# Performance work log

Measured on AMD Instinct MI355X. Metric: run time of the kernel, lower is better.

## Reference

```python
import jax, jax.numpy as jnp
import numpy as np

DIM = 96
HEADS = 3
WS = (2, 7, 7)   # window (Wt, Wh, Ww)
SS = (1, 3, 3)   # shift (St, Sh, Sw)
MLP_H = 4 * DIM
B, T, H, W = 1, 16, 112, 112
EPS = 1e-5


def _partition(x, ws):
    # (b,t,h,w,c) -> (b * t/Wt * h/Wh * w/Ww, Wt*Wh*Ww, c); works for np and jnp
    b, t, h, w, c = x.shape
    Wt, Wh, Ww = ws
    x = x.reshape(b, t // Wt, Wt, h // Wh, Wh, w // Ww, Ww, c)
    return x.transpose(0, 1, 3, 5, 2, 4, 6, 7).reshape(-1, Wt * Wh * Ww, c)


def _reverse(win, ws, b, t, h, w):
    Wt, Wh, Ww = ws
    c = win.shape[-1]
    x = win.reshape(b, t // Wt, h // Wh, w // Ww, Wt, Wh, Ww, c)
    return x.transpose(0, 1, 4, 2, 5, 3, 6, 7).reshape(b, t, h, w, c)


def _rel_pos_index(ws):
    Wt, Wh, Ww = ws
    coords = np.stack(np.meshgrid(np.arange(Wt), np.arange(Wh), np.arange(Ww), indexing='ij'))
    cf = coords.reshape(3, -1)
    rel = (cf[:, :, None] - cf[:, None, :]).transpose(1, 2, 0).astype(np.int64)
    rel[..., 0] += Wt - 1
    rel[..., 1] += Wh - 1
    rel[..., 2] += Ww - 1
    rel[..., 0] *= (2 * Wh - 1) * (2 * Ww - 1)
    rel[..., 1] *= 2 * Ww - 1
    return jnp.asarray(rel.sum(-1))  # (N, N)


def _attn_mask(tp, hp, wp, ws, ss):
    img = np.zeros((1, tp, hp, wp, 1), np.float32)
    cnt = 0
    def sl(Wd, Sd):
        return (slice(0, -Wd), slice(-Wd, -Sd), slice(-Sd, None))
    for ts in sl(ws[0], ss[0]):
        for hs in sl(ws[1], ss[1]):
            for wws in sl(ws[2], ss[2]):
                img[:, ts, hs, wws, :] = cnt
                cnt += 1
    mw = _partition(img, ws)[..., 0]                 # (nW, N)
    am = mw[:, None, :] - mw[:, :, None]
    return jnp.asarray(np.where(am != 0, -100.0, 0.0).astype(np.float32))


def _ln(x, g, b):
    m = x.mean(-1, keepdims=True)
    v = ((x - m) ** 2).mean(-1, keepdims=True)
    return (x - m) * jax.lax.rsqrt(v + EPS) * g + b


def setup_inputs() -> dict:
    key = jax.random.key(0)
    ks = jax.random.split(key, 8)
    Wt, Wh, Ww = WS
    n_bias = (2 * Wt - 1) * (2 * Wh - 1) * (2 * Ww - 1)
    s = 0.02
    return {
        'x': jax.random.normal(ks[0], (B, T, H, W, DIM), jnp.float32),
        'g1': jnp.ones((DIM,), jnp.float32),
        'b1': jnp.zeros((DIM,), jnp.float32),
        'qkv_w': jax.random.normal(ks[1], (DIM, 3 * DIM), jnp.float32) * s,
        'qkv_b': jnp.zeros((3 * DIM,), jnp.float32),
        'rpb': jax.random.normal(ks[2], (n_bias, HEADS), jnp.float32) * s,
        'proj_w': jax.random.normal(ks[3], (DIM, DIM), jnp.float32) * s,
        'proj_b': jnp.zeros((DIM,), jnp.float32),
        'g2': jnp.ones((DIM,), jnp.float32),
        'b2': jnp.zeros((DIM,), jnp.float32),
        'fc1_w': jax.random.normal(ks[4], (DIM, MLP_H), jnp.float32) * s,
        'fc1_b': jnp.zeros((MLP_H,), jnp.float32),
        'fc2_w': jax.random.normal(ks[5], (MLP_H, DIM), jnp.float32) * s,
        'fc2_b': jnp.zeros((DIM,), jnp.float32),
    }


def reference(x, g1, b1, qkv_w, qkv_b, rpb, proj_w, proj_b, g2, b2, fc1_w, fc1_b, fc2_w, fc2_b):
    Wt, Wh, Ww = WS
    St, Sh, Sw = SS
    Bx, Tx, Hx, Wx, C = x.shape
    N = Wt * Wh * Ww
    hd = C // HEADS
    shortcut = x
    xn = _ln(x, g1, b1)
    xs = jnp.roll(xn, (-St, -Sh, -Sw), axis=(1, 2, 3))
    xw = _partition(xs, WS)                           # (B_, N, C)
    B_ = xw.shape[0]
    nW = B_ // Bx
    qkv = (xw @ qkv_w + qkv_b).reshape(B_, N, 3, HEADS, hd).transpose(2, 0, 3, 1, 4)
    q, k, v = qkv[0] * (hd ** -0.5), qkv[1], qkv[2]   # (B_, H, N, hd)
    attn = jnp.einsum('bhnd,bhmd->bhnm', q, k)
    ridx = _rel_pos_index(WS)
    bias = rpb[ridx.reshape(-1)].reshape(N, N, HEADS).transpose(2, 0, 1)
    attn = attn + bias[None]
    mask = _attn_mask(Tx, Hx, Wx, WS, SS)             # (nW, N, N)
    attn = attn.reshape(Bx, nW, HEADS, N, N) + mask[None, :, None]
    attn = jax.nn.softmax(attn.reshape(B_, HEADS, N, N), axis=-1)
    out = jnp.einsum('bhnm,bhmd->bhnd', attn, v).transpose(0, 2, 1, 3).reshape(B_, N, C)
    out = out @ proj_w + proj_b
    xr = _reverse(out, WS, Bx, Tx, Hx, Wx)
    xr = jnp.roll(xr, (St, Sh, Sw), axis=(1, 2, 3))
    x1 = shortcut + xr
    xn2 = _ln(x1, g2, b2)
    h1 = jax.nn.gelu(xn2 @ fc1_w + fc1_b, approximate=False)
    return x1 + h1 @ fc2_w + fc2_b
```

## Files before the change

kernel.cpp:

```cpp
#include <hip/hip_runtime.h>
#include <math.h>

#define TT 16
#define HH 112
#define WD 112
#define CC 96
#define NHEADS 3
#define HD 32
#define NN 98
#define NWIN 2048
#define NTOK 200704
#define MLPH 384
#define SXP 104
#define SQP 40
#define SVP 136
#define SHP 392
#define SX1P 100

typedef unsigned int  u32;
typedef unsigned short u16;
typedef float f32x4 __attribute__((ext_vector_type(4)));
typedef short bf16x8 __attribute__((ext_vector_type(8)));

__device__ inline u16 f2bf(float f) {
  u32 u = __float_as_uint(f);
  u += 0x7fffu + ((u >> 16) & 1u);
  return (u16)(u >> 16);
}
__device__ inline float bflo(u32 u) { return __uint_as_float(u << 16); }
__device__ inline float bfhi(u32 u) { return __uint_as_float(u & 0xffff0000u); }

#define MFMA16(a, b, c) __builtin_amdgcn_mfma_f32_16x16x32_bf16((a), (b), (c), 0, 0, 0)

__global__ __launch_bounds__(256) void wprep_kernel(
    const float* __restrict__ qkv_w, const float* __restrict__ proj_w,
    const float* __restrict__ fc1_w, const float* __restrict__ fc2_w,
    u16* __restrict__ qkv_wT, u16* __restrict__ proj_wT,
    u16* __restrict__ fc1_wT, u16* __restrict__ fc2_wT) {
  int idx = blockIdx.x * 256 + threadIdx.x;
  if (idx < 27648) {
    int col = idx / CC, c = idx - col * CC;
    qkv_wT[idx] = f2bf(qkv_w[c * (3 * CC) + col]);
    return;
  }
  idx -= 27648;
  if (idx < 9216) {
    int col = idx / CC, c = idx - col * CC;
    proj_wT[idx] = f2bf(proj_w[c * CC + col]);
    return;
  }
  idx -= 9216;
  if (idx < 36864) {
    int j = idx / CC, c = idx - j * CC;
    fc1_wT[idx] = f2bf(fc1_w[c * MLPH + j]);
    return;
  }
  idx -= 36864;
  if (idx < 36864) {
    int c = idx / MLPH, j = idx - c * MLPH;
    fc2_wT[idx] = f2bf(fc2_w[j * CC + c]);
  }
}

__global__ __launch_bounds__(256) void bias_kernel(const float* __restrict__ rpb,
                                                   float* __restrict__ biasTP) {
  int idx = blockIdx.x * 256 + threadIdx.x;
  if (idx >= NHEADS * 112 * 128) return;
  int head = idx / (112 * 128);
  int r = idx - head * 112 * 128;
  int q = r / 128, kv = r - q * 128;
  float v;
  if (kv >= NN) v = -30000.f;
  else if (q >= NN) v = 0.f;
  else {
    int itq = q / 49, rq = q - itq * 49, ihq = rq / 7, iwq = rq - ihq * 7;
    int itk = kv / 49, rk = kv - itk * 49, ihk = rk / 7, iwk = rk - ihk * 7;
    int ridx = (itq - itk + 1) * 169 + (ihq - ihk + 6) * 13 + (iwq - iwk + 6);
    v = rpb[ridx * NHEADS + head];
  }
  biasTP[idx] = v;
}

__global__ __launch_bounds__(256) void ln1_kernel(
    const float* __restrict__ x, const float* __restrict__ g1, const float* __restrict__ b1,
    u16* __restrict__ xnw)
{
  const int tid = threadIdx.x;
  const int row = blockIdx.x * 64 + (tid >> 2);
  const int qd = tid & 3;
  const int widx = row / 112;
  const int n = row - widx * 112;
  u16* dst = xnw + (size_t)row * CC + qd * 24;
  if (n >= NN) {
    uint4 z = {0u, 0u, 0u, 0u};
    *(uint4*)(dst) = z; *(uint4*)(dst + 8) = z; *(uint4*)(dst + 16) = z;
    return;
  }
  int it = n / 49, r = n - it * 49, ih = r / 7, iw = r - ih * 7;
  int ww = widx & 15, hw = (widx >> 4) & 15, tw = widx >> 8;
  int t = tw * 2 + it + 1; if (t >= TT) t -= TT;
  int h = hw * 7 + ih + 3; if (h >= HH) h -= HH;
  int w = ww * 7 + iw + 3; if (w >= WD) w -= WD;
  const float* src = x + ((size_t)(t * HH + h) * WD + w) * CC + qd * 24;
  float v[24];
  #pragma unroll
  for (int i = 0; i < 24; i += 4) {
    float4 f = *(const float4*)(src + i);
    v[i] = f.x; v[i + 1] = f.y; v[i + 2] = f.z; v[i + 3] = f.w;
  }
  float sm = 0.f;
  #pragma unroll
  for (int i = 0; i < 24; ++i) sm += v[i];
  sm += __shfl_xor(sm, 1, 64);
  sm += __shfl_xor(sm, 2, 64);
  float mu = sm * (1.f / CC);
  float sq = 0.f;
  #pragma unroll
  for (int i = 0; i < 24; ++i) { float d = v[i] - mu; sq += d * d; }
  sq += __shfl_xor(sq, 1, 64);
  sq += __shfl_xor(sq, 2, 64);
  float inv = rsqrtf(sq * (1.f / CC) + 1e-5f);
  u16 o[24];
  #pragma unroll
  for (int i = 0; i < 24; ++i) {
    int c = qd * 24 + i;
    o[i] = f2bf((v[i] - mu) * inv * g1[c] + b1[c]);
  }
  *(uint4*)(dst)      = *(const uint4*)(o);
  *(uint4*)(dst + 8)  = *(const uint4*)(o + 8);
  *(uint4*)(dst + 16) = *(const uint4*)(o + 16);
}

__global__ __launch_bounds__(256, 4) void attn_kernel(
    const u16* __restrict__ xnw, const u16* __restrict__ qkv_wT, const float* __restrict__ qkv_b,
    const float* __restrict__ biasTP, u16* __restrict__ att)
{
  __shared__ __align__(16) u16 sUni[112 * SVP];
  __shared__ __align__(16) u16 sVt[32 * SVP];
  __shared__ int sReg[112];

  u16* sQ = sUni;
  u16* sK = sUni + 112 * SQP;
  u16* sP = sUni;

  const int tid  = threadIdx.x;
  const int bid  = blockIdx.x;
  const int widx = bid / 3;
  const int head = bid - widx * 3;
  const int ww = widx & 15, hw = (widx >> 4) & 15, tw = widx >> 8;
  const bool bnd = (tw == 7) || (hw == 15) || (ww == 15);
  const int wid = tid >> 6;
  const int lane = tid & 63;
  const int g  = lane >> 4;
  const int cl = lane & 15;
  const int mt1ok = (wid + 4) < 7;

  bf16x8 xa[2][3];
  {
    const u16* arow0 = xnw + ((size_t)widx * 112 + wid * 16 + cl) * CC + 8 * g;
    xa[0][0] = *(const bf16x8*)(arow0);
    xa[0][1] = *(const bf16x8*)(arow0 + 32);
    xa[0][2] = *(const bf16x8*)(arow0 + 64);
    const int mtb = mt1ok ? (wid + 4) : wid;
    const u16* arow1 = xnw + ((size_t)widx * 112 + mtb * 16 + cl) * CC + 8 * g;
    xa[1][0] = *(const bf16x8*)(arow1);
    xa[1][1] = *(const bf16x8*)(arow1 + 32);
    xa[1][2] = *(const bf16x8*)(arow1 + 64);
  }

  for (int i = tid; i < 32 * SVP / 2; i += 256) ((u32*)sVt)[i] = 0;
  if (tid < 112) {
    int n = tid;
    int reg = 0;
    if (n < NN) {
      int it = n / 49, r = n - it * 49, ih = r / 7, iw = r - ih * 7;
      int ts = tw * 2 + it, hs = hw * 7 + ih, ws2 = ww * 7 + iw;
      int rt = ts < TT - 2 ? 0 : (ts < TT - 1 ? 1 : 2);
      int rh = hs < HH - 7 ? 0 : (hs < HH - 3 ? 1 : 2);
      int rw = ws2 < WD - 7 ? 0 : (ws2 < WD - 3 ? 1 : 2);
      reg = rt * 9 + rh * 3 + rw;
    }
    sReg[n] = reg;
  }
  __syncthreads();

  {
    const float scale = 0.17677669529663687f;
    #pragma unroll
    for (int nt = 0; nt < 6; ++nt) {
      const int sec = nt >> 1;
      const int col = sec * 96 + head * 32 + (nt & 1) * 16 + cl;
      const u16* brow = qkv_wT + (size_t)col * CC + 8 * g;
      bf16x8 b0 = *(const bf16x8*)(brow);
      bf16x8 b1 = *(const bf16x8*)(brow + 32);
      bf16x8 b2 = *(const bf16x8*)(brow + 64);
      const float bias = qkv_b[col];
      #pragma unroll
      for (int mi = 0; mi < 2; ++mi) {
        const int mt = wid + mi * 4;
        if (mi == 1 && !mt1ok) continue;
        f32x4 acc = {0.f, 0.f, 0.f, 0.f};
        acc = MFMA16(xa[mi][0], b0, acc);
        acc = MFMA16(xa[mi][1], b1, acc);
        acc = MFMA16(xa[mi][2], b2, acc);
        #pragma unroll
        for (int r = 0; r < 4; ++r) {
          const int row = mt * 16 + 4 * g + r;
          const float v = acc[r] + bias;
          if (sec == 0)      sQ[row * SQP + (nt & 1) * 16 + cl] = f2bf(v * scale);
          else if (sec == 1) sK[row * SQP + (nt & 1) * 16 + cl] = f2bf(v);
          else               sVt[((nt & 1) * 16 + cl) * SVP + row] = f2bf(v);
        }
      }
    }
  }
  __syncthreads();

  float sv[2][7][4];
  #pragma unroll
  for (int mi = 0; mi < 2; ++mi) {
    const int mt = wid + mi * 4;
    if (mt >= 7) continue;
    const int q0 = mt * 16 + 4 * g;
    bf16x8 a = *(const bf16x8*)&sQ[(mt * 16 + cl) * SQP + 8 * g];
    __builtin_amdgcn_s_setprio(1);
    #pragma unroll
    for (int nt = 0; nt < 7; ++nt) {
      bf16x8 b = *(const bf16x8*)&sK[(nt * 16 + cl) * SQP + 8 * g];
      const float* bp = biasTP + ((size_t)(head * 112 + q0) * 128 + nt * 16 + cl);
      f32x4 acc = {bp[0], bp[128], bp[256], bp[384]};
      acc = MFMA16(a, b, acc);
      #pragma unroll
      for (int r = 0; r < 4; ++r) sv[mi][nt][r] = acc[r];
    }
    __builtin_amdgcn_s_setprio(0);
    if (bnd) {
      #pragma unroll
      for (int nt = 0; nt < 7; ++nt) {
        const int kv = nt * 16 + cl;
        #pragma unroll
        for (int r = 0; r < 4; ++r) {
          if (sReg[q0 + r] != sReg[kv]) sv[mi][nt][r] -= 100.f;
        }
      }
    }
    #pragma unroll
    for (int r = 0; r < 4; ++r) {
      float mx = sv[mi][0][r];
      #pragma unroll
      for (int nt = 1; nt < 7; ++nt) mx = fmaxf(mx, sv[mi][nt][r]);
      #pragma unroll
      for (int d = 1; d < 16; d <<= 1) mx = fmaxf(mx, __shfl_xor(mx, d, 64));
      float sm = 0.f;
      #pragma unroll
      for (int nt = 0; nt < 7; ++nt) { float p = __expf(sv[mi][nt][r] - mx); sv[mi][nt][r] = p; sm += p; }
      #pragma unroll
      for (int d = 1; d < 16; d <<= 1) sm += __shfl_xor(sm, d, 64);
      const float inv = 1.f / sm;
      #pragma unroll
      for (int nt = 0; nt < 7; ++nt) sv[mi][nt][r] *= inv;
    }
  }
  __syncthreads();

  #pragma unroll
  for (int mi = 0; mi < 2; ++mi) {
    const int mt = wid + mi * 4;
    if (mt >= 7) continue;
    #pragma unroll
    for (int r = 0; r < 4; ++r) {
      const int q = mt * 16 + 4 * g + r;
      u16* prow = &sP[q * SVP];
      #pragma unroll
      for (int nt = 0; nt < 7; ++nt) prow[nt * 16 + cl] = f2bf(sv[mi][nt][r]);
      prow[112 + cl] = 0;
    }
  }
  __syncthreads();

  for (int t = wid; t < 14; t += 4) {
    const int mt = t >> 1, ntd = t & 1;
    f32x4 acc = {0.f, 0.f, 0.f, 0.f};
    __builtin_amdgcn_s_setprio(1);
    #pragma unroll
    for (int ks = 0; ks < 4; ++ks) {
      bf16x8 a = *(const bf16x8*)&sP[(mt * 16 + cl) * SVP + ks * 32 + 8 * g];
      bf16x8 b = *(const bf16x8*)&sVt[(ntd * 16 + cl) * SVP + ks * 32 + 8 * g];
      acc = MFMA16(a, b, acc);
    }
    __builtin_amdgcn_s_setprio(0);
    #pragma unroll
    for (int r = 0; r < 4; ++r) {
      const int q = mt * 16 + 4 * g + r;
      if (q < NN)
        att[((size_t)widx * NN + q) * CC + head * 32 + ntd * 16 + cl] = f2bf(acc[r]);
    }
  }
}

__global__ __launch_bounds__(128, 4) void pm_kernel(
    const u16* __restrict__ att, const u16* __restrict__ proj_wT, const float* __restrict__ proj_b,
    const float* __restrict__ x,
    const float* __restrict__ g2, const float* __restrict__ b2,
    const u16* __restrict__ fc1_wT, const float* __restrict__ fc1_b,
    const u16* __restrict__ fc2_wT, const float* __restrict__ fc2_b,
    float* __restrict__ out)
{
  __shared__ __align__(16) u16 sH [32 * SHP];
  __shared__ __align__(16) u16 sXn[32 * SXP];

  u16* sA  = sH;
  u16* sX1 = sH + 4096;

  const int tid  = threadIdx.x;
  const int base = blockIdx.x * 32;
  const int hnt  = tid >> 6;
  const int lane = tid & 63, g = lane >> 4, cl = lane & 15;

  u32 nr[2][4];
  #pragma unroll
  for (int mt = 0; mt < 2; ++mt) {
    #pragma unroll
    for (int r = 0; r < 4; ++r) {
      int tok = base + mt * 16 + 4 * g + r;
      int widx = tok / NN, n = tok - widx * NN;
      int ww = widx & 15, hw = (widx >> 4) & 15, tw = widx >> 8;
      int it = n / 49, rr = n - it * 49, ih = rr / 7, iw = rr - ih * 7;
      int t = tw * 2 + it + 1; if (t >= TT) t -= TT;
      int h = hw * 7 + ih + 3; if (h >= HH) h -= HH;
      int w = ww * 7 + iw + 3; if (w >= WD) w -= WD;
      nr[mt][r] = (u32)((t * HH + h) * WD + w);
    }
  }
  float xres[3][2][4];
  #pragma unroll
  for (int j = 0; j < 3; ++j) {
    const int col = (hnt * 3 + j) * 16 + cl;
    #pragma unroll
    for (int mt = 0; mt < 2; ++mt)
      #pragma unroll
      for (int r = 0; r < 4; ++r)
        xres[j][mt][r] = x[(size_t)nr[mt][r] * CC + col];
  }

  for (int e = tid; e < 32 * 12; e += 128) {
    int tok = e / 12, kb = e - tok * 12;
    *(uint4*)&sA[tok * SXP + kb * 8] =
        ((const uint4*)att)[(size_t)(base + tok) * 12 + kb];
  }
  __syncthreads();

  float x1v[3][2][4];
  {
    bf16x8 a[2][3];
    #pragma unroll
    for (int mt = 0; mt < 2; ++mt) {
      const u16* aRow = &sA[(mt * 16 + cl) * SXP + 8 * g];
      a[mt][0] = *(const bf16x8*)(aRow);
      a[mt][1] = *(const bf16x8*)(aRow + 32);
      a[mt][2] = *(const bf16x8*)(aRow + 64);
    }
    #pragma unroll
    for (int j = 0; j < 3; ++j) {
      const int nt = hnt * 3 + j;
      const u16* bRow = proj_wT + (nt * 16 + cl) * CC + 8 * g;
      bf16x8 b0 = *(const bf16x8*)(bRow);
      bf16x8 b1 = *(const bf16x8*)(bRow + 32);
      bf16x8 b2 = *(const bf16x8*)(bRow + 64);
      const float bc = proj_b[nt * 16 + cl];
      #pragma unroll
      for (int mt = 0; mt < 2; ++mt) {
        f32x4 acc = {0.f, 0.f, 0.f, 0.f};
        acc = MFMA16(a[mt][0], b0, acc);
        acc = MFMA16(a[mt][1], b1, acc);
        acc = MFMA16(a[mt][2], b2, acc);
        #pragma unroll
        for (int r = 0; r < 4; ++r) {
          const int row = mt * 16 + 4 * g + r;
          const float v = acc[r] + bc + xres[j][mt][r];
          x1v[j][mt][r] = v;
          sX1[row * SX1P + nt * 16 + cl] = f2bf(v);
        }
      }
    }
  }
  __syncthreads();

  {
    const int tok = tid >> 2, sub = tid & 3;
    const u16* p = &sX1[tok * SX1P + sub * 24];
    float v[24];
    #pragma unroll
    for (int k = 0; k < 12; ++k) {
      u32 u = *(const u32*)(p + 2 * k);
      v[2 * k] = bflo(u); v[2 * k + 1] = bfhi(u);
    }
    float sm = 0.f;
    #pragma unroll
    for (int i = 0; i < 24; ++i) sm += v[i];
    sm += __shfl_xor(sm, 1, 64);
    sm += __shfl_xor(sm, 2, 64);
    float mu = sm * (1.f / CC);
    float sq = 0.f;
    #pragma unroll
    for (int i = 0; i < 24; ++i) { float d = v[i] - mu; sq += d * d; }
    sq += __shfl_xor(sq, 1, 64);
    sq += __shfl_xor(sq, 2, 64);
    float inv = rsqrtf(sq * (1.f / CC) + 1e-5f);
    u16 o[24];
    #pragma unroll
    for (int i = 0; i < 24; ++i) {
      int c = sub * 24 + i;
      o[i] = f2bf((v[i] - mu) * inv * g2[c] + b2[c]);
    }
    u16* dst = &sXn[tok * SXP + sub * 24];
    *(uint4*)(dst)      = *(const uint4*)(o);
    *(uint4*)(dst + 8)  = *(const uint4*)(o + 8);
    *(uint4*)(dst + 16) = *(const uint4*)(o + 16);
  }
  __syncthreads();

  {
    bf16x8 a[2][3];
    #pragma unroll
    for (int mt = 0; mt < 2; ++mt) {
      const u16* aXn = &sXn[(mt * 16 + cl) * SXP + 8 * g];
      a[mt][0] = *(const bf16x8*)(aXn);
      a[mt][1] = *(const bf16x8*)(aXn + 32);
      a[mt][2] = *(const bf16x8*)(aXn + 64);
    }
    const int nt0 = hnt * 12;
    const u16* bPtr = fc1_wT + ((size_t)(nt0 * 16 + cl)) * CC + 8 * g;
    bf16x8 b0 = *(const bf16x8*)(bPtr);
    bf16x8 b1 = *(const bf16x8*)(bPtr + 32);
    bf16x8 b2 = *(const bf16x8*)(bPtr + 64);
    #pragma unroll
    for (int j = 0; j < 12; ++j) {
      bf16x8 c0 = b0, c1 = b1, c2 = b2;
      if (j < 11) {
        bPtr += 16 * CC;
        b0 = *(const bf16x8*)(bPtr);
        b1 = *(const bf16x8*)(bPtr + 32);
        b2 = *(const bf16x8*)(bPtr + 64);
      }
      const int nt = nt0 + j;
      const float bj = fc1_b[nt * 16 + cl];
      #pragma unroll
      for (int mt = 0; mt < 2; ++mt) {
        f32x4 acc = {0.f, 0.f, 0.f, 0.f};
        acc = MFMA16(a[mt][0], c0, acc);
        acc = MFMA16(a[mt][1], c1, acc);
        acc = MFMA16(a[mt][2], c2, acc);
        #pragma unroll
        for (int r = 0; r < 4; ++r) {
          float v = acc[r] + bj;
          float p2 = v * v;
          float aa = v * fmaf(0.07135481f, p2, 1.59576912f);
          float e  = __expf(aa);
          float gl = v * e * __builtin_amdgcn_rcpf(e + 1.f);
          sH[(mt * 16 + 4 * g + r) * SHP + nt * 16 + cl] = f2bf(gl);
        }
      }
    }
  }
  __syncthreads();

  {
    f32x4 acc2[3][2];
    #pragma unroll
    for (int j = 0; j < 3; ++j)
      #pragma unroll
      for (int mt = 0; mt < 2; ++mt) { f32x4 z = {0.f, 0.f, 0.f, 0.f}; acc2[j][mt] = z; }

    #pragma unroll
    for (int q = 0; q < 4; ++q) {
      bf16x8 a[2][3];
      #pragma unroll
      for (int mt = 0; mt < 2; ++mt) {
        const u16* aBase = &sH[(mt * 16 + cl) * SHP + q * 96 + 8 * g];
        a[mt][0] = *(const bf16x8*)(aBase);
        a[mt][1] = *(const bf16x8*)(aBase + 32);
        a[mt][2] = *(const bf16x8*)(aBase + 64);
      }
      #pragma unroll
      for (int j = 0; j < 3; ++j) {
        const int nt = hnt * 3 + j;
        const u16* bBase = fc2_wT + (size_t)(nt * 16 + cl) * MLPH + q * 96 + 8 * g;
        bf16x8 b0 = *(const bf16x8*)(bBase);
        bf16x8 b1 = *(const bf16x8*)(bBase + 32);
        bf16x8 b2 = *(const bf16x8*)(bBase + 64);
        #pragma unroll
        for (int mt = 0; mt < 2; ++mt) {
          acc2[j][mt] = MFMA16(a[mt][0], b0, acc2[j][mt]);
          acc2[j][mt] = MFMA16(a[mt][1], b1, acc2[j][mt]);
          acc2[j][mt] = MFMA16(a[mt][2], b2, acc2[j][mt]);
        }
      }
    }
    #pragma unroll
    for (int j = 0; j < 3; ++j) {
      const int nt = hnt * 3 + j;
      const float bc = fc2_b[nt * 16 + cl];
      #pragma unroll
      for (int mt = 0; mt < 2; ++mt)
        #pragma unroll
        for (int r = 0; r < 4; ++r)
          out[(size_t)nr[mt][r] * CC + nt * 16 + cl] = x1v[j][mt][r] + acc2[j][mt][r] + bc;
    }
  }
}

extern "C" void kernel_launch(void* const* d_in, const int* in_sizes, int n_in,
                              void* d_out, int out_size, void* d_ws, size_t ws_size,
                              hipStream_t stream) {
  const float* x      = (const float*)d_in[0];
  const float* g1     = (const float*)d_in[1];
  const float* b1     = (const float*)d_in[2];
  const float* qkv_w  = (const float*)d_in[3];
  const float* qkv_b  = (const float*)d_in[4];
  const float* rpb    = (const float*)d_in[5];
  const float* proj_w = (const float*)d_in[6];
  const float* proj_b = (const float*)d_in[7];
  const float* g2     = (const float*)d_in[8];
  const float* b2     = (const float*)d_in[9];
  const float* fc1_w  = (const float*)d_in[10];
  const float* fc1_b  = (const float*)d_in[11];
  const float* fc2_w  = (const float*)d_in[12];
  const float* fc2_b  = (const float*)d_in[13];

  char* ws = (char*)d_ws;
  u16*   att    = (u16*)ws;
  u16*   xnw    = (u16*)(ws + (size_t)NTOK * CC * 2);
  char*  wtail  = ws + (size_t)NTOK * CC * 2 + (size_t)NWIN * 112 * CC * 2;
  float* biasTP = (float*)wtail;
  u16*   qkv_wT = (u16*)(wtail + 172032);
  u16*   proj_wT= (u16*)(wtail + 172032 + 55296);
  u16*   fc1_wT = (u16*)(wtail + 172032 + 55296 + 18432);
  u16*   fc2_wT = (u16*)(wtail + 172032 + 55296 + 18432 + 73728);

  wprep_kernel<<<(27648 + 9216 + 36864 + 36864 + 255) / 256, 256, 0, stream>>>(
      qkv_w, proj_w, fc1_w, fc2_w, qkv_wT, proj_wT, fc1_wT, fc2_wT);
  bias_kernel<<<(NHEADS * 112 * 128 + 255) / 256, 256, 0, stream>>>(rpb, biasTP);
  ln1_kernel<<<NWIN * 112 / 64, 256, 0, stream>>>(x, g1, b1, xnw);
  attn_kernel<<<NWIN * NHEADS, 256, 0, stream>>>(xnw, qkv_wT, qkv_b, biasTP, att);
  pm_kernel<<<NTOK / 32, 128, 0, stream>>>(att, proj_wT, proj_b, x, g2, b2,
                                           fc1_wT, fc1_b, fc2_wT, fc2_b, (float*)d_out);
}
```

Measured before the change: 212.3 us.

## Split MLP hidden into two halves to shrink LDS and load attention directly

The fused proj+MLP kernel now computes fc1+GELU for half of the 384 hidden units at a time into a 192-wide LDS buffer, then accumulates fc2 over that half before processing the second half. This halves the hidden-activation LDS footprint. The attention-output tile is now read straight from global memory into MFMA registers instead of being staged through LDS, which removes one barrier. The trade-offs are an extra barrier per half, larger register arrays for the fc2 A operands, and lowering the launch-bounds occupancy hint from 4 to 3 blocks per SM, which may cut resident waves.

After: 249.7 us. 1.18x slower.

```diff
diff --git a/kernel.cpp b/kernel.cpp
--- a/kernel.cpp
+++ b/kernel.cpp
@@ -14,7 +14,7 @@
 #define SXP 104
 #define SQP 40
 #define SVP 136
-#define SHP 392
+#define SH2P 200
 #define SX1P 100
 
 typedef unsigned int  u32;
@@ -298,7 +298,7 @@
   }
 }
 
-__global__ __launch_bounds__(128, 4) void pm_kernel(
+__global__ __launch_bounds__(128, 3) void pm_kernel(
     const u16* __restrict__ att, const u16* __restrict__ proj_wT, const float* __restrict__ proj_b,
     const float* __restrict__ x,
     const float* __restrict__ g2, const float* __restrict__ b2,
@@ -306,11 +306,9 @@
     const u16* __restrict__ fc2_wT, const float* __restrict__ fc2_b,
     float* __restrict__ out)
 {
-  __shared__ __align__(16) u16 sH [32 * SHP];
+  __shared__ __align__(16) u16 sHh[32 * SH2P];
+  __shared__ __align__(16) u16 sX1[32 * SX1P];
   __shared__ __align__(16) u16 sXn[32 * SXP];
-
-  u16* sA  = sH;
-  u16* sX1 = sH + 4096;
 
   const int tid  = threadIdx.x;
   const int base = blockIdx.x * 32;
@@ -343,19 +341,12 @@
         xres[j][mt][r] = x[(size_t)nr[mt][r] * CC + col];
   }
 
-  for (int e = tid; e < 32 * 12; e += 128) {
-    int tok = e / 12, kb = e - tok * 12;
-    *(uint4*)&sA[tok * SXP + kb * 8] =
-        ((const uint4*)att)[(size_t)(base + tok) * 12 + kb];
-  }
-  __syncthreads();
-
   float x1v[3][2][4];
   {
     bf16x8 a[2][3];
     #pragma unroll
     for (int mt = 0; mt < 2; ++mt) {
-      const u16* aRow = &sA[(mt * 16 + cl) * SXP + 8 * g];
+      const u16* aRow = att + (size_t)(base + mt * 16 + cl) * CC + 8 * g;
       a[mt][0] = *(const bf16x8*)(aRow);
       a[mt][1] = *(const bf16x8*)(aRow + 32);
       a[mt][2] = *(const bf16x8*)(aRow + 64);
@@ -420,93 +411,93 @@
   }
   __syncthreads();
 
-  {
-    bf16x8 a[2][3];
-    #pragma unroll
-    for (int mt = 0; mt < 2; ++mt) {
-      const u16* aXn = &sXn[(mt * 16 + cl) * SXP + 8 * g];
-      a[mt][0] = *(const bf16x8*)(aXn);
-      a[mt][1] = *(const bf16x8*)(aXn + 32);
-      a[mt][2] = *(const bf16x8*)(aXn + 64);
-    }
-    const int nt0 = hnt * 12;
-    const u16* bPtr = fc1_wT + ((size_t)(nt0 * 16 + cl)) * CC + 8 * g;
-    bf16x8 b0 = *(const bf16x8*)(bPtr);
-    bf16x8 b1 = *(const bf16x8*)(bPtr + 32);
-    bf16x8 b2 = *(const bf16x8*)(bPtr + 64);
-    #pragma unroll
-    for (int j = 0; j < 12; ++j) {
-      bf16x8 c0 = b0, c1 = b1, c2 = b2;
-      if (j < 11) {
-        bPtr += 16 * CC;
-        b0 = *(const bf16x8*)(bPtr);
-        b1 = *(const bf16x8*)(bPtr + 32);
-        b2 = *(const bf16x8*)(bPtr + 64);
-      }
-      const int nt = nt0 + j;
-      const float bj = fc1_b[nt * 16 + cl];
-      #pragma unroll
-      for (int mt = 0; mt < 2; ++mt) {
-        f32x4 acc = {0.f, 0.f, 0.f, 0.f};
-        acc = MFMA16(a[mt][0], c0, acc);
-        acc = MFMA16(a[mt][1], c1, acc);
-        acc = MFMA16(a[mt][2], c2, acc);
+  f32x4 acc2[3][2];
+  #pragma unroll
+  for (int j = 0; j < 3; ++j)
+    #pragma unroll
+    for (int mt = 0; mt < 2; ++mt) { f32x4 z = {0.f, 0.f, 0.f, 0.f}; acc2[j][mt] = z; }
+
+  bf16x8 aXn[2][3];
+  #pragma unroll
+  for (int mt = 0; mt < 2; ++mt) {
+    const u16* ap = &sXn[(mt * 16 + cl) * SXP + 8 * g];
+    aXn[mt][0] = *(const bf16x8*)(ap);
+    aXn[mt][1] = *(const bf16x8*)(ap + 32);
+    aXn[mt][2] = *(const bf16x8*)(ap + 64);
+  }
+
+  #pragma unroll
+  for (int hf = 0; hf < 2; ++hf) {
+    {
+      const int nt0 = hf * 12 + hnt * 6;
+      const u16* bPtr = fc1_wT + ((size_t)(nt0 * 16 + cl)) * CC + 8 * g;
+      bf16x8 b0 = *(const bf16x8*)(bPtr);
+      bf16x8 b1 = *(const bf16x8*)(bPtr + 32);
+      bf16x8 b2 = *(const bf16x8*)(bPtr + 64);
+      #pragma unroll
+      for (int j = 0; j < 6; ++j) {
+        bf16x8 c0 = b0, c1 = b1, c2 = b2;
+        if (j < 5) {
+          bPtr += 16 * CC;
+          b0 = *(const bf16x8*)(bPtr);
+          b1 = *(const bf16x8*)(bPtr + 32);
+          b2 = *(const bf16x8*)(bPtr + 64);
+        }
+        const int nt = nt0 + j;
+        const float bj = fc1_b[nt * 16 + cl];
+        const int lcol = (hnt * 6 + j) * 16 + cl;
         #pragma unroll
-        for (int r = 0; r < 4; ++r) {
-          float v = acc[r] + bj;
-          float p2 = v * v;
-          float aa = v * fmaf(0.07135481f, p2, 1.59576912f);
-          float e  = __expf(aa);
-          float gl = v * e * __builtin_amdgcn_rcpf(e + 1.f);
-          sH[(mt * 16 + 4 * g + r) * SHP + nt * 16 + cl] = f2bf(gl);
+        for (int mt = 0; mt < 2; ++mt) {
+          f32x4 acc = {0.f, 0.f, 0.f, 0.f};
+          acc = MFMA16(aXn[mt][0], c0, acc);
+          acc = MFMA16(aXn[mt][1], c1, acc);
+          acc = MFMA16(aXn[mt][2], c2, acc);
+          #pragma unroll
+          for (int r = 0; r < 4; ++r) {
+            float v = acc[r] + bj;
+            float p2 = v * v;
+            float aa = v * fmaf(0.07135481f, p2, 1.59576912f);
+            float e  = __expf(aa);
+            float gl = v * e * __builtin_amdgcn_rcpf(e + 1.f);
+            sHh[(mt * 16 + 4 * g + r) * SH2P + lcol] = f2bf(gl);
+          }
         }
       }
     }
-  }
-  __syncthreads();
-
-  {
-    f32x4 acc2[3][2];
-    #pragma unroll
-    for (int j = 0; j < 3; ++j)
-      #pragma unroll
-      for (int mt = 0; mt < 2; ++mt) { f32x4 z = {0.f, 0.f, 0.f, 0.f}; acc2[j][mt] = z; }
-
-    #pragma unroll
-    for (int q = 0; q < 4; ++q) {
-      bf16x8 a[2][3];
+    __syncthreads();
+    {
+      bf16x8 a[2][6];
       #pragma unroll
       for (int mt = 0; mt < 2; ++mt) {
-        const u16* aBase = &sH[(mt * 16 + cl) * SHP + q * 96 + 8 * g];
-        a[mt][0] = *(const bf16x8*)(aBase);
-        a[mt][1] = *(const bf16x8*)(aBase + 32);
-        a[mt][2] = *(const bf16x8*)(aBase + 64);
+        const u16* aBase = &sHh[(mt * 16 + cl) * SH2P + 8 * g];
+        #pragma unroll
+        for (int ks = 0; ks < 6; ++ks) a[mt][ks] = *(const bf16x8*)(aBase + 32 * ks);
       }
       #pragma unroll
       for (int j = 0; j < 3; ++j) {
         const int nt = hnt * 3 + j;
-        const u16* bBase = fc2_wT + (size_t)(nt * 16 + cl) * MLPH + q * 96 + 8 * g;
-        bf16x8 b0 = *(const bf16x8*)(bBase);
-        bf16x8 b1 = *(const bf16x8*)(bBase + 32);
-        bf16x8 b2 = *(const bf16x8*)(bBase + 64);
+        const u16* bBase = fc2_wT + (size_t)(nt * 16 + cl) * MLPH + hf * 192 + 8 * g;
         #pragma unroll
-        for (int mt = 0; mt < 2; ++mt) {
-          acc2[j][mt] = MFMA16(a[mt][0], b0, acc2[j][mt]);
-          acc2[j][mt] = MFMA16(a[mt][1], b1, acc2[j][mt]);
-          acc2[j][mt] = MFMA16(a[mt][2], b2, acc2[j][mt]);
+        for (int ks = 0; ks < 6; ++ks) {
+          bf16x8 b = *(const bf16x8*)(bBase + 32 * ks);
+          #pragma unroll
+          for (int mt = 0; mt < 2; ++mt)
+            acc2[j][mt] = MFMA16(a[mt][ks], b, acc2[j][mt]);
         }
       }
     }
-    #pragma unroll
-    for (int j = 0; j < 3; ++j) {
-      const int nt = hnt * 3 + j;
-      const float bc = fc2_b[nt * 16 + cl];
-      #pragma unroll
-      for (int mt = 0; mt < 2; ++mt)
-        #pragma unroll
-        for (int r = 0; r < 4; ++r)
-          out[(size_t)nr[mt][r] * CC + nt * 16 + cl] = x1v[j][mt][r] + acc2[j][mt][r] + bc;
-    }
+    if (hf == 0) __syncthreads();
+  }
+
+  #pragma unroll
+  for (int j = 0; j < 3; ++j) {
+    const int nt = hnt * 3 + j;
+    const float bc = fc2_b[nt * 16 + cl];
+    #pragma unroll
+    for (int mt = 0; mt < 2; ++mt)
+      #pragma unroll
+      for (int r = 0; r < 4; ++r)
+        out[(size_t)nr[mt][r] * CC + nt * 16 + cl] = x1v[j][mt][r] + acc2[j][mt][r] + bc;
   }
 }
 
```
